# Optimization experiments

Hardware: AMD Instinct MI355X
Metric: run time of the kernel (lower is better)

Reference implementation:

```python
import jax, jax.numpy as jnp
import numpy as np
import math

B, S, T, F_IN, D = 4, 4096, 4096, 127, 64

def setup_inputs() -> dict:
    key = jax.random.key(0)
    k1, k2, k3, k4 = jax.random.split(key, 4)
    return {
        "x1": jax.random.normal(k1, (B, S, F_IN), dtype=jnp.float32),
        "x2": jax.random.normal(k2, (B, T, F_IN), dtype=jnp.float32),
        "W": jax.random.normal(k3, (D, F_IN), dtype=jnp.float32) * (1.0 / math.sqrt(F_IN)),
        "b": jax.random.normal(k4, (D,), dtype=jnp.float32) * 0.01,
    }

def reference(x1, x2, W, b):
    # shared linear projection: torch Linear -> x @ W.T + b
    q = jnp.einsum('bsf,df->bsd', x1, W) + b   # [B,S,D]
    k = jnp.einsum('btf,df->btd', x2, W) + b   # [B,T,D]
    scores = jnp.einsum('bsd,btd->bst', q, k)  # [B,S,T]
    # faithful to source: v4 = v3.div(1/sqrt(D)) == v3 * sqrt(D)
    scores = scores * jnp.sqrt(jnp.float32(D))
    p = jax.nn.softmax(scores, axis=-1)        # [B,S,T]
    # dropout p=0.01 treated as eval-mode identity (deterministic reference)
    out = jnp.einsum('bst,btf->bsf', p, x2)    # [B,S,F_IN]
    return out
```

## Files before the change

### kernel.cpp

```cpp
#include <hip/hip_runtime.h>
#include <hip/hip_bf16.h>


typedef __bf16 bf16x8 __attribute__((ext_vector_type(8)));
typedef float f32x16 __attribute__((ext_vector_type(16)));

#define S_DIM 4096
#define F_DIM 127
#define QSCALE 11.5415603271f
#define THR 11.0f

static __device__ __forceinline__ unsigned short f2bf(float f) {
  unsigned u = __float_as_uint(f);
  unsigned r = u + 0x7FFFu + ((u >> 16) & 1u);
  return (unsigned short)(r >> 16);
}
static __device__ __forceinline__ float bf2f(unsigned short h) {
  return __uint_as_float(((unsigned)h) << 16);
}
static __device__ __forceinline__ unsigned cvt_pk_bf16(float lo, float hi) {
  unsigned r;
  asm("v_cvt_pk_bf16_f32 %0, %1, %2" : "=v"(r) : "v"(lo), "v"(hi));
  return r;
}
static __device__ __forceinline__ float exp2_fast(float x) {
  float r;
  asm("v_exp_f32 %0, %1" : "=v"(r) : "v"(x));
  return r;
}
static __device__ __forceinline__ bf16x8 mk_bf16x8(unsigned w0, unsigned w1,
                                                   unsigned w2, unsigned w3) {
  unsigned t[4] = {w0, w1, w2, w3};
  bf16x8 r;
  __builtin_memcpy(&r, t, 16);
  return r;
}
static __device__ __forceinline__ bf16x8 u4_bf16x8(uint4 v) {
  bf16x8 r;
  __builtin_memcpy(&r, &v, 16);
  return r;
}

__global__ __launch_bounds__(256) void proj_kernel(
    const float* __restrict__ x1, const float* __restrict__ x2,
    const float* __restrict__ W, const float* __restrict__ bias,
    float* __restrict__ Qf, uint4* __restrict__ khf, uint4* __restrict__ klf) {
  __shared__ unsigned kstage[4][32 * 66];
  const int tid = threadIdx.x;
  const int wave = tid >> 6;
  const int lane = tid & 63;
  const int arow = lane & 31;
  const int half = lane >> 5;
  const int bi = blockIdx.x;
  const bool isK = bi >= 128;
  const float* x = isK ? x2 : x1;
  const int grow0 = (bi & 127) * 128 + wave * 32;
  const float* xrow = x + (long)(grow0 + arow) * F_DIM;

  bf16x8 xh[8], xl[8];
#pragma unroll
  for (int kk = 0; kk < 8; ++kk) {
    unsigned short hs[8], ls[8];
#pragma unroll
    for (int j = 0; j < 8; ++j) {
      const int f = kk * 16 + half * 8 + j;
      const float v = (f < F_DIM) ? xrow[f] : 0.f;
      const unsigned short h = f2bf(v);
      hs[j] = h;
      ls[j] = f2bf(v - bf2f(h));
    }
    __builtin_memcpy(&xh[kk], hs, 16);
    __builtin_memcpy(&xl[kk], ls, 16);
  }

  f32x16 acc0, acc1;
#pragma unroll
  for (int r = 0; r < 16; ++r) {
    acc0[r] = 0.f;
    acc1[r] = 0.f;
  }

  const float* wr0 = W + (long)arow * F_DIM;
  const float* wr1 = W + (long)(32 + arow) * F_DIM;
#pragma unroll
  for (int kk = 0; kk < 8; ++kk) {
    unsigned short h0[8], l0[8], h1[8], l1[8];
#pragma unroll
    for (int j = 0; j < 8; ++j) {
      const int f = kk * 16 + half * 8 + j;
      const float v0 = (f < F_DIM) ? wr0[f] : 0.f;
      const float v1 = (f < F_DIM) ? wr1[f] : 0.f;
      const unsigned short a = f2bf(v0);
      h0[j] = a;
      l0[j] = f2bf(v0 - bf2f(a));
      const unsigned short c = f2bf(v1);
      h1[j] = c;
      l1[j] = f2bf(v1 - bf2f(c));
    }
    bf16x8 wh0, wl0, wh1, wl1;
    __builtin_memcpy(&wh0, h0, 16);
    __builtin_memcpy(&wl0, l0, 16);
    __builtin_memcpy(&wh1, h1, 16);
    __builtin_memcpy(&wl1, l1, 16);
    acc0 = __builtin_amdgcn_mfma_f32_32x32x16_bf16(xh[kk], wh0, acc0, 0, 0, 0);
    acc0 = __builtin_amdgcn_mfma_f32_32x32x16_bf16(xh[kk], wl0, acc0, 0, 0, 0);
    acc0 = __builtin_amdgcn_mfma_f32_32x32x16_bf16(xl[kk], wh0, acc0, 0, 0, 0);
    acc1 = __builtin_amdgcn_mfma_f32_32x32x16_bf16(xh[kk], wh1, acc1, 0, 0, 0);
    acc1 = __builtin_amdgcn_mfma_f32_32x32x16_bf16(xh[kk], wl1, acc1, 0, 0, 0);
    acc1 = __builtin_amdgcn_mfma_f32_32x32x16_bf16(xl[kk], wh1, acc1, 0, 0, 0);
  }

  unsigned* kst = kstage[wave];
#pragma unroll
  for (int dt = 0; dt < 2; ++dt) {
    const f32x16 acc = dt ? acc1 : acc0;
    const int d = dt * 32 + arow;
    const float bd = bias[d];
#pragma unroll
    for (int r = 0; r < 16; ++r) {
      const int row = (r & 3) + 8 * (r >> 2) + 4 * half;
      const float val = acc[r] + bd;
      if (!isK) {
        Qf[(long)(grow0 + row) * 64 + d] = val * QSCALE;
      } else {
        const unsigned short h = f2bf(val);
        const unsigned short lo = f2bf(val - bf2f(h));
        kst[row * 66 + d] = (unsigned)h | ((unsigned)lo << 16);
      }
    }
  }

  if (isK) {
    const int b = grow0 >> 12;
    const int tile = (grow0 & (S_DIM - 1)) >> 5;
    uint4* ko = khf + ((long)(b * 128 + tile) * 4) * 64 + lane;
    uint4* lo_ = klf + ((long)(b * 128 + tile) * 4) * 64 + lane;
#pragma unroll
    for (int kk = 0; kk < 4; ++kk) {
      const int d0 = kk * 16 + half * 8;
      unsigned w[8];
#pragma unroll
      for (int j = 0; j < 8; ++j) w[j] = kst[arow * 66 + d0 + j];
      unsigned hw[4], lw[4];
#pragma unroll
      for (int g = 0; g < 4; ++g) {
        hw[g] = (w[2 * g] & 0xffffu) | (w[2 * g + 1] << 16);
        lw[g] = (w[2 * g] >> 16) | (w[2 * g + 1] & 0xffff0000u);
      }
      ko[kk * 64] = make_uint4(hw[0], hw[1], hw[2], hw[3]);
      lo_[kk * 64] = make_uint4(lw[0], lw[1], lw[2], lw[3]);
    }
  }
}

__global__ __launch_bounds__(256) void x2repack_kernel(
    const float* __restrict__ x2, uint4* __restrict__ x2tf) {
  const int tid = threadIdx.x;
  const int bi = blockIdx.x;
  const int b = bi >> 8;
  const int tt = bi & 255;
  const int fb = tid >> 6;
  const int l = tid & 63;
  const int t0 = tt * 16 + ((l >> 5) << 3);
  const int f = fb * 32 + (l & 31);
  const float* src = x2 + ((long)b * S_DIM + t0) * F_DIM + f;
  unsigned short e[8];
#pragma unroll
  for (int j = 0; j < 8; ++j)
    e[j] = (f < F_DIM) ? f2bf(src[(long)j * F_DIM]) : (unsigned short)0;
  unsigned w0 = (unsigned)e[0] | ((unsigned)e[1] << 16);
  unsigned w1 = (unsigned)e[2] | ((unsigned)e[3] << 16);
  unsigned w2 = (unsigned)e[4] | ((unsigned)e[5] << 16);
  unsigned w3 = (unsigned)e[6] | ((unsigned)e[7] << 16);
  x2tf[((long)(b * 256 + tt) * 4 + fb) * 64 + l] = make_uint4(w0, w1, w2, w3);
}

__global__ __launch_bounds__(256, 2) void attn_kernel(
    const float* __restrict__ Qf, const uint4* __restrict__ khf,
    const uint4* __restrict__ klf, const uint4* __restrict__ x2tf,
    float* __restrict__ out) {
  const int tid = threadIdx.x;
  const int lane = tid & 63;
  const int wave = tid >> 6;
  const int col = lane & 31;
  const int half = lane >> 5;
  const int bi = blockIdx.x;
  const int b = bi >> 7;
  const int q0 = (bi & 127) << 5;

  bf16x8 qh[4], ql[4];
  {
    const float* qrow = Qf + ((long)(b * S_DIM + q0 + col)) * 64;
#pragma unroll
    for (int kk = 0; kk < 4; ++kk) {
      const int d0 = kk * 16 + half * 8;
      unsigned short hs[8], ls[8];
#pragma unroll
      for (int j = 0; j < 8; ++j) {
        const float qv = qrow[d0 + j];
        const unsigned short h = f2bf(qv);
        hs[j] = h;
        ls[j] = f2bf(qv - bf2f(h));
      }
      __builtin_memcpy(&qh[kk], hs, 16);
      __builtin_memcpy(&ql[kk], ls, 16);
    }
  }

  const uint4* khfp = khf + (long)b * 128 * 4 * 64;
  const uint4* klfp = klf + (long)b * 128 * 4 * 64;
  const uint4* xfp = x2tf + (long)b * 256 * 4 * 64;

  f32x16 a0, a1, a2, a3;
#pragma unroll
  for (int r = 0; r < 16; ++r) {
    a0[r] = 0.f; a1[r] = 0.f; a2[r] = 0.f; a3[r] = 0.f;
  }
  float m = -INFINITY;
  float lsum = 0.f;

  uint4 KC[8], KN[8];
#pragma unroll
  for (int kk = 0; kk < 4; ++kk) {
    KC[kk] = khfp[(wave * 4 + kk) * 64 + lane];
    KC[4 + kk] = klfp[(wave * 4 + kk) * 64 + lane];
  }

#pragma unroll 2
  for (int it = 0; it < 32; ++it) {
    const int tile = (it << 2) + wave;
    uint4 xv[8];
#pragma unroll
    for (int kf = 0; kf < 2; ++kf)
#pragma unroll
      for (int fb = 0; fb < 4; ++fb)
        xv[kf * 4 + fb] = xfp[((tile * 2 + kf) * 4 + fb) * 64 + lane];
    int tn = tile + 4;
    if (tn > 127) tn = 127;
#pragma unroll
    for (int kk = 0; kk < 4; ++kk) {
      KN[kk] = khfp[(tn * 4 + kk) * 64 + lane];
      KN[4 + kk] = klfp[(tn * 4 + kk) * 64 + lane];
    }
    f32x16 st;
#pragma unroll
    for (int r = 0; r < 16; ++r) st[r] = 0.f;
#pragma unroll
    for (int kk = 0; kk < 4; ++kk) {
      const bf16x8 kv = u4_bf16x8(KC[kk]);
      const bf16x8 lv = u4_bf16x8(KC[4 + kk]);
      st = __builtin_amdgcn_mfma_f32_32x32x16_bf16(kv, qh[kk], st, 0, 0, 0);
      st = __builtin_amdgcn_mfma_f32_32x32x16_bf16(kv, ql[kk], st, 0, 0, 0);
      st = __builtin_amdgcn_mfma_f32_32x32x16_bf16(lv, qh[kk], st, 0, 0, 0);
    }
    float pmax = st[0];
#pragma unroll
    for (int r = 1; r < 16; ++r) pmax = fmaxf(pmax, st[r]);
    pmax = fmaxf(pmax, __shfl_xor(pmax, 32));
    if (__any(pmax > m + THR)) {
      const float mnew = fmaxf(m, pmax);
      const float sc = exp2_fast(m - mnew);
      lsum *= sc;
#pragma unroll
      for (int r = 0; r < 16; ++r) {
        a0[r] *= sc; a1[r] *= sc; a2[r] *= sc; a3[r] *= sc;
      }
      m = mnew;
    }
    float ts = 0.f;
    unsigned pg[4][2];
#pragma unroll
    for (int g = 0; g < 4; ++g) {
      const float p0 = exp2_fast(st[4 * g + 0] - m);
      const float p1 = exp2_fast(st[4 * g + 1] - m);
      const float p2 = exp2_fast(st[4 * g + 2] - m);
      const float p3 = exp2_fast(st[4 * g + 3] - m);
      ts += (p0 + p1) + (p2 + p3);
      pg[g][0] = cvt_pk_bf16(p0, p1);
      pg[g][1] = cvt_pk_bf16(p2, p3);
    }
    lsum += ts;
#pragma unroll
    for (int kk = 0; kk < 2; ++kk) {
      unsigned x0 = pg[2 * kk][0], y0 = pg[2 * kk + 1][0];
      unsigned x1 = pg[2 * kk][1], y1 = pg[2 * kk + 1][1];
      asm("v_permlane32_swap_b32 %0, %1" : "+v"(x0), "+v"(y0));
      asm("v_permlane32_swap_b32 %0, %1" : "+v"(x1), "+v"(y1));
      const bf16x8 pf = mk_bf16x8(x0, x1, y0, y1);
      a0 = __builtin_amdgcn_mfma_f32_32x32x16_bf16(u4_bf16x8(xv[kk * 4 + 0]),
                                                   pf, a0, 0, 0, 0);
      a1 = __builtin_amdgcn_mfma_f32_32x32x16_bf16(u4_bf16x8(xv[kk * 4 + 1]),
                                                   pf, a1, 0, 0, 0);
      a2 = __builtin_amdgcn_mfma_f32_32x32x16_bf16(u4_bf16x8(xv[kk * 4 + 2]),
                                                   pf, a2, 0, 0, 0);
      a3 = __builtin_amdgcn_mfma_f32_32x32x16_bf16(u4_bf16x8(xv[kk * 4 + 3]),
                                                   pf, a3, 0, 0, 0);
    }
#pragma unroll
    for (int i = 0; i < 8; ++i) KC[i] = KN[i];
  }
  lsum += __shfl_xor(lsum, 32);

  __shared__ float mbuf[4][32];
  __shared__ float lbuf[4][32];
  __shared__ float accbuf[128 * 33];
  if (lane < 32) {
    mbuf[wave][col] = m;
    lbuf[wave][col] = lsum;
  }
  __syncthreads();
  const float mstar = fmaxf(fmaxf(mbuf[0][col], mbuf[1][col]),
                            fmaxf(mbuf[2][col], mbuf[3][col]));
  const float wsc = exp2_fast(m - mstar);
  for (int w = 0; w < 4; ++w) {
    if (wave == w) {
#pragma unroll
      for (int fb = 0; fb < 4; ++fb) {
        const f32x16 av = (fb == 0) ? a0 : (fb == 1) ? a1 : (fb == 2) ? a2 : a3;
#pragma unroll
        for (int r = 0; r < 16; ++r) {
          const int f = fb * 32 + (r & 3) + 8 * (r >> 2) + 4 * half;
          const float v = av[r] * wsc;
          if (w == 0) accbuf[f * 33 + col] = v;
          else accbuf[f * 33 + col] += v;
        }
      }
    }
    __syncthreads();
  }
  const int q = tid >> 3;
  const int fg = tid & 7;
  const float ms2 = fmaxf(fmaxf(mbuf[0][q], mbuf[1][q]),
                          fmaxf(mbuf[2][q], mbuf[3][q]));
  float lst = 0.f;
#pragma unroll
  for (int w = 0; w < 4; ++w) lst += lbuf[w][q] * exp2_fast(mbuf[w][q] - ms2);
  const float inv = 1.0f / lst;
  float* ob = out + ((long)(b * S_DIM + q0 + q)) * F_DIM;
#pragma unroll
  for (int j = 0; j < 16; ++j) {
    const int f = fg * 16 + j;
    if (f < F_DIM) ob[f] = accbuf[f * 33 + q] * inv;
  }
}

extern "C" void kernel_launch(void* const* d_in, const int* in_sizes, int n_in,
                              void* d_out, int out_size, void* d_ws,
                              size_t ws_size, hipStream_t stream) {
  const float* x1 = (const float*)d_in[0];
  const float* x2 = (const float*)d_in[1];
  const float* W = (const float*)d_in[2];
  const float* bias = (const float*)d_in[3];
  float* out = (float*)d_out;

  char* ws = (char*)d_ws;
  float* Qf = (float*)ws;
  uint4* khf = (uint4*)(ws + (4l << 20));
  uint4* klf = (uint4*)(ws + (6l << 20));
  uint4* x2tf = (uint4*)(ws + (8l << 20));

  hipLaunchKernelGGL(proj_kernel, dim3(256), dim3(256), 0, stream, x1, x2, W,
                     bias, Qf, khf, klf);
  hipLaunchKernelGGL(x2repack_kernel, dim3(1024), dim3(256), 0, stream, x2,
                     x2tf);
  hipLaunchKernelGGL(attn_kernel, dim3(512), dim3(256), 0, stream, Qf, khf,
                     klf, x2tf, out);
}
```

Before: 76.45 us.

## Prepack W and Q fragments, fold softmax sum into padding column, widen attention blocks

A new kernel pre-splits W into hi/lo bf16 MFMA fragments, stored in the output buffer as scratch, so the projection no longer converts W per block. Q is now written as pre-packed hi/lo bf16 fragments, which removes the per-block split in the attention kernel. The row-sum of probabilities is dropped from the loop: the padded 128th feature column of x2 is set to 1.0, so the PV MFMA computes the denominator for free. The attention kernel uses 512-thread blocks covering 64 queries with an XCD-aware block remap and register double-buffering of K. Together these cut VALU work and conversions, at the cost of a larger reduction LDS footprint and an extra launch.

```diff
diff --git a/kernel.cpp b/kernel.cpp
--- a/kernel.cpp
+++ b/kernel.cpp
@@ -10,14 +10,6 @@
 #define QSCALE 11.5415603271f
 #define THR 11.0f
 
-static __device__ __forceinline__ unsigned short f2bf(float f) {
-  unsigned u = __float_as_uint(f);
-  unsigned r = u + 0x7FFFu + ((u >> 16) & 1u);
-  return (unsigned short)(r >> 16);
-}
-static __device__ __forceinline__ float bf2f(unsigned short h) {
-  return __uint_as_float(((unsigned)h) << 16);
-}
 static __device__ __forceinline__ unsigned cvt_pk_bf16(float lo, float hi) {
   unsigned r;
   asm("v_cvt_pk_bf16_f32 %0, %1, %2" : "=v"(r) : "v"(lo), "v"(hi));
@@ -41,10 +33,36 @@
   return r;
 }
 
+__global__ __launch_bounds__(256) void wfrag_kernel(const float* __restrict__ W,
+                                                    uint4* __restrict__ wf) {
+  const int gid = blockIdx.x * 256 + threadIdx.x;
+  const int dt = gid >> 9;
+  const int kk = (gid >> 6) & 7;
+  const int lane = gid & 63;
+  const int d = dt * 32 + (lane & 31);
+  const int f0b = kk * 16 + (lane >> 5) * 8;
+  const float* wr = W + (long)d * F_DIM;
+  unsigned hw[4], lw[4];
+#pragma unroll
+  for (int g = 0; g < 4; ++g) {
+    const int f0 = f0b + 2 * g;
+    const float v0 = (f0 < F_DIM) ? wr[f0] : 0.f;
+    const float v1 = (f0 + 1 < F_DIM) ? wr[f0 + 1] : 0.f;
+    const unsigned h = cvt_pk_bf16(v0, v1);
+    const float l0 = v0 - __uint_as_float(h << 16);
+    const float l1 = v1 - __uint_as_float(h & 0xffff0000u);
+    hw[g] = h;
+    lw[g] = cvt_pk_bf16(l0, l1);
+  }
+  wf[((dt * 8 + kk) * 64 + lane) * 2 + 0] = make_uint4(hw[0], hw[1], hw[2], hw[3]);
+  wf[((dt * 8 + kk) * 64 + lane) * 2 + 1] = make_uint4(lw[0], lw[1], lw[2], lw[3]);
+}
+
 __global__ __launch_bounds__(256) void proj_kernel(
     const float* __restrict__ x1, const float* __restrict__ x2,
-    const float* __restrict__ W, const float* __restrict__ bias,
-    float* __restrict__ Qf, uint4* __restrict__ khf, uint4* __restrict__ klf) {
+    const uint4* __restrict__ wf, const float* __restrict__ bias,
+    uint4* __restrict__ qhf, uint4* __restrict__ qlf,
+    uint4* __restrict__ khf, uint4* __restrict__ klf) {
   __shared__ unsigned kstage[4][32 * 66];
   const int tid = threadIdx.x;
   const int wave = tid >> 6;
@@ -60,17 +78,20 @@
   bf16x8 xh[8], xl[8];
 #pragma unroll
   for (int kk = 0; kk < 8; ++kk) {
-    unsigned short hs[8], ls[8];
-#pragma unroll
-    for (int j = 0; j < 8; ++j) {
-      const int f = kk * 16 + half * 8 + j;
-      const float v = (f < F_DIM) ? xrow[f] : 0.f;
-      const unsigned short h = f2bf(v);
-      hs[j] = h;
-      ls[j] = f2bf(v - bf2f(h));
-    }
-    __builtin_memcpy(&xh[kk], hs, 16);
-    __builtin_memcpy(&xl[kk], ls, 16);
+    unsigned hw[4], lw[4];
+#pragma unroll
+    for (int g = 0; g < 4; ++g) {
+      const int f0 = kk * 16 + half * 8 + 2 * g;
+      const float v0 = (f0 < F_DIM) ? xrow[f0] : 0.f;
+      const float v1 = (f0 + 1 < F_DIM) ? xrow[f0 + 1] : 0.f;
+      const unsigned h = cvt_pk_bf16(v0, v1);
+      const float l0 = v0 - __uint_as_float(h << 16);
+      const float l1 = v1 - __uint_as_float(h & 0xffff0000u);
+      hw[g] = h;
+      lw[g] = cvt_pk_bf16(l0, l1);
+    }
+    xh[kk] = mk_bf16x8(hw[0], hw[1], hw[2], hw[3]);
+    xl[kk] = mk_bf16x8(lw[0], lw[1], lw[2], lw[3]);
   }
 
   f32x16 acc0, acc1;
@@ -79,29 +100,12 @@
     acc0[r] = 0.f;
     acc1[r] = 0.f;
   }
-
-  const float* wr0 = W + (long)arow * F_DIM;
-  const float* wr1 = W + (long)(32 + arow) * F_DIM;
 #pragma unroll
   for (int kk = 0; kk < 8; ++kk) {
-    unsigned short h0[8], l0[8], h1[8], l1[8];
-#pragma unroll
-    for (int j = 0; j < 8; ++j) {
-      const int f = kk * 16 + half * 8 + j;
-      const float v0 = (f < F_DIM) ? wr0[f] : 0.f;
-      const float v1 = (f < F_DIM) ? wr1[f] : 0.f;
-      const unsigned short a = f2bf(v0);
-      h0[j] = a;
-      l0[j] = f2bf(v0 - bf2f(a));
-      const unsigned short c = f2bf(v1);
-      h1[j] = c;
-      l1[j] = f2bf(v1 - bf2f(c));
-    }
-    bf16x8 wh0, wl0, wh1, wl1;
-    __builtin_memcpy(&wh0, h0, 16);
-    __builtin_memcpy(&wl0, l0, 16);
-    __builtin_memcpy(&wh1, h1, 16);
-    __builtin_memcpy(&wl1, l1, 16);
+    const bf16x8 wh0 = u4_bf16x8(wf[((0 * 8 + kk) * 64 + lane) * 2 + 0]);
+    const bf16x8 wl0 = u4_bf16x8(wf[((0 * 8 + kk) * 64 + lane) * 2 + 1]);
+    const bf16x8 wh1 = u4_bf16x8(wf[((1 * 8 + kk) * 64 + lane) * 2 + 0]);
+    const bf16x8 wl1 = u4_bf16x8(wf[((1 * 8 + kk) * 64 + lane) * 2 + 1]);
     acc0 = __builtin_amdgcn_mfma_f32_32x32x16_bf16(xh[kk], wh0, acc0, 0, 0, 0);
     acc0 = __builtin_amdgcn_mfma_f32_32x32x16_bf16(xh[kk], wl0, acc0, 0, 0, 0);
     acc0 = __builtin_amdgcn_mfma_f32_32x32x16_bf16(xl[kk], wh0, acc0, 0, 0, 0);
@@ -117,39 +121,41 @@
     const int d = dt * 32 + arow;
     const float bd = bias[d];
 #pragma unroll
-    for (int r = 0; r < 16; ++r) {
-      const int row = (r & 3) + 8 * (r >> 2) + 4 * half;
-      const float val = acc[r] + bd;
+    for (int r = 0; r < 16; r += 2) {
+      const int row0 = (r & 3) + 8 * (r >> 2) + 4 * half;
+      float v0 = acc[r] + bd;
+      float v1 = acc[r + 1] + bd;
       if (!isK) {
-        Qf[(long)(grow0 + row) * 64 + d] = val * QSCALE;
-      } else {
-        const unsigned short h = f2bf(val);
-        const unsigned short lo = f2bf(val - bf2f(h));
-        kst[row * 66 + d] = (unsigned)h | ((unsigned)lo << 16);
+        v0 *= QSCALE;
+        v1 *= QSCALE;
       }
-    }
-  }
-
-  if (isK) {
-    const int b = grow0 >> 12;
-    const int tile = (grow0 & (S_DIM - 1)) >> 5;
-    uint4* ko = khf + ((long)(b * 128 + tile) * 4) * 64 + lane;
-    uint4* lo_ = klf + ((long)(b * 128 + tile) * 4) * 64 + lane;
-#pragma unroll
-    for (int kk = 0; kk < 4; ++kk) {
-      const int d0 = kk * 16 + half * 8;
-      unsigned w[8];
-#pragma unroll
-      for (int j = 0; j < 8; ++j) w[j] = kst[arow * 66 + d0 + j];
-      unsigned hw[4], lw[4];
-#pragma unroll
-      for (int g = 0; g < 4; ++g) {
-        hw[g] = (w[2 * g] & 0xffffu) | (w[2 * g + 1] << 16);
-        lw[g] = (w[2 * g] >> 16) | (w[2 * g + 1] & 0xffff0000u);
-      }
-      ko[kk * 64] = make_uint4(hw[0], hw[1], hw[2], hw[3]);
-      lo_[kk * 64] = make_uint4(lw[0], lw[1], lw[2], lw[3]);
-    }
+      const unsigned h = cvt_pk_bf16(v0, v1);
+      const float l0 = v0 - __uint_as_float(h << 16);
+      const float l1 = v1 - __uint_as_float(h & 0xffff0000u);
+      const unsigned l = cvt_pk_bf16(l0, l1);
+      kst[row0 * 66 + d] = (h & 0xffffu) | (l << 16);
+      kst[(row0 + 1) * 66 + d] = (h >> 16) | (l & 0xffff0000u);
+    }
+  }
+
+  const int b = grow0 >> 12;
+  const int tile = (grow0 & (S_DIM - 1)) >> 5;
+  uint4* dh = (isK ? khf : qhf) + ((long)(b * 128 + tile) * 4) * 64 + lane;
+  uint4* dl = (isK ? klf : qlf) + ((long)(b * 128 + tile) * 4) * 64 + lane;
+#pragma unroll
+  for (int kk = 0; kk < 4; ++kk) {
+    const int d0 = kk * 16 + half * 8;
+    unsigned w[8];
+#pragma unroll
+    for (int j = 0; j < 8; ++j) w[j] = kst[arow * 66 + d0 + j];
+    unsigned hw[4], lw[4];
+#pragma unroll
+    for (int g = 0; g < 4; ++g) {
+      hw[g] = (w[2 * g] & 0xffffu) | (w[2 * g + 1] << 16);
+      lw[g] = (w[2 * g] >> 16) | (w[2 * g + 1] & 0xffff0000u);
+    }
+    dh[kk * 64] = make_uint4(hw[0], hw[1], hw[2], hw[3]);
+    dl[kk * 64] = make_uint4(lw[0], lw[1], lw[2], lw[3]);
   }
 }
 
@@ -164,47 +170,40 @@
   const int t0 = tt * 16 + ((l >> 5) << 3);
   const int f = fb * 32 + (l & 31);
   const float* src = x2 + ((long)b * S_DIM + t0) * F_DIM + f;
-  unsigned short e[8];
-#pragma unroll
-  for (int j = 0; j < 8; ++j)
-    e[j] = (f < F_DIM) ? f2bf(src[(long)j * F_DIM]) : (unsigned short)0;
-  unsigned w0 = (unsigned)e[0] | ((unsigned)e[1] << 16);
-  unsigned w1 = (unsigned)e[2] | ((unsigned)e[3] << 16);
-  unsigned w2 = (unsigned)e[4] | ((unsigned)e[5] << 16);
-  unsigned w3 = (unsigned)e[6] | ((unsigned)e[7] << 16);
-  x2tf[((long)(b * 256 + tt) * 4 + fb) * 64 + l] = make_uint4(w0, w1, w2, w3);
-}
-
-__global__ __launch_bounds__(256, 2) void attn_kernel(
-    const float* __restrict__ Qf, const uint4* __restrict__ khf,
-    const uint4* __restrict__ klf, const uint4* __restrict__ x2tf,
-    float* __restrict__ out) {
+  unsigned w[4];
+#pragma unroll
+  for (int g = 0; g < 4; ++g) {
+    const float v0 = (f < F_DIM) ? src[(long)(2 * g) * F_DIM] : 1.0f;
+    const float v1 = (f < F_DIM) ? src[(long)(2 * g + 1) * F_DIM] : 1.0f;
+    w[g] = cvt_pk_bf16(v0, v1);
+  }
+  x2tf[((long)(b * 256 + tt) * 4 + fb) * 64 + l] = make_uint4(w[0], w[1], w[2], w[3]);
+}
+
+__global__ __launch_bounds__(512, 2) void attn_kernel(
+    const uint4* __restrict__ qhf, const uint4* __restrict__ qlf,
+    const uint4* __restrict__ khf, const uint4* __restrict__ klf,
+    const uint4* __restrict__ x2tf, float* __restrict__ out) {
   const int tid = threadIdx.x;
   const int lane = tid & 63;
   const int wave = tid >> 6;
   const int col = lane & 31;
   const int half = lane >> 5;
+  const int sub = wave & 1;
+  const int qtr = wave >> 1;
   const int bi = blockIdx.x;
-  const int b = bi >> 7;
-  const int q0 = (bi & 127) << 5;
-
+  const int xcd = bi & 7;
+  const int slot = bi >> 3;
+  const int L = (xcd >> 1) * 64 + slot * 2 + (xcd & 1);
+  const int b = L >> 6;
+  const int q0 = (L & 63) << 6;
+
+  const int qtile = ((q0 + sub * 32) & (S_DIM - 1)) >> 5;
   bf16x8 qh[4], ql[4];
-  {
-    const float* qrow = Qf + ((long)(b * S_DIM + q0 + col)) * 64;
-#pragma unroll
-    for (int kk = 0; kk < 4; ++kk) {
-      const int d0 = kk * 16 + half * 8;
-      unsigned short hs[8], ls[8];
-#pragma unroll
-      for (int j = 0; j < 8; ++j) {
-        const float qv = qrow[d0 + j];
-        const unsigned short h = f2bf(qv);
-        hs[j] = h;
-        ls[j] = f2bf(qv - bf2f(h));
-      }
-      __builtin_memcpy(&qh[kk], hs, 16);
-      __builtin_memcpy(&ql[kk], ls, 16);
-    }
+#pragma unroll
+  for (int kk = 0; kk < 4; ++kk) {
+    qh[kk] = u4_bf16x8(qhf[((long)(b * 128 + qtile) * 4 + kk) * 64 + lane]);
+    ql[kk] = u4_bf16x8(qlf[((long)(b * 128 + qtile) * 4 + kk) * 64 + lane]);
   }
 
   const uint4* khfp = khf + (long)b * 128 * 4 * 64;
@@ -217,38 +216,40 @@
     a0[r] = 0.f; a1[r] = 0.f; a2[r] = 0.f; a3[r] = 0.f;
   }
   float m = -INFINITY;
-  float lsum = 0.f;
-
-  uint4 KC[8], KN[8];
-#pragma unroll
-  for (int kk = 0; kk < 4; ++kk) {
-    KC[kk] = khfp[(wave * 4 + kk) * 64 + lane];
-    KC[4 + kk] = klfp[(wave * 4 + kk) * 64 + lane];
-  }
-
-#pragma unroll 2
-  for (int it = 0; it < 32; ++it) {
-    const int tile = (it << 2) + wave;
+
+  uint4 KA[8], KB[8];
+  {
+    const int t0_ = qtr;
+#pragma unroll
+    for (int kk = 0; kk < 4; ++kk) {
+      KA[kk] = khfp[(t0_ * 4 + kk) * 64 + lane];
+      KA[4 + kk] = klfp[(t0_ * 4 + kk) * 64 + lane];
+    }
+  }
+
+  auto body = [&](const uint4 (&C)[8], uint4 (&N)[8], int i) {
+    const int tile = (i << 2) + qtr;
     uint4 xv[8];
 #pragma unroll
     for (int kf = 0; kf < 2; ++kf)
 #pragma unroll
       for (int fb = 0; fb < 4; ++fb)
         xv[kf * 4 + fb] = xfp[((tile * 2 + kf) * 4 + fb) * 64 + lane];
-    int tn = tile + 4;
-    if (tn > 127) tn = 127;
+    if (i < 31) {
+      const int tn = ((i + 1) << 2) + qtr;
+#pragma unroll
+      for (int kk = 0; kk < 4; ++kk) {
+        N[kk] = khfp[(tn * 4 + kk) * 64 + lane];
+        N[4 + kk] = klfp[(tn * 4 + kk) * 64 + lane];
+      }
+    }
+    f32x16 st;
+#pragma unroll
+    for (int r = 0; r < 16; ++r) st[r] = 0.f;
 #pragma unroll
     for (int kk = 0; kk < 4; ++kk) {
-      KN[kk] = khfp[(tn * 4 + kk) * 64 + lane];
-      KN[4 + kk] = klfp[(tn * 4 + kk) * 64 + lane];
-    }
-    f32x16 st;
-#pragma unroll
-    for (int r = 0; r < 16; ++r) st[r] = 0.f;
-#pragma unroll
-    for (int kk = 0; kk < 4; ++kk) {
-      const bf16x8 kv = u4_bf16x8(KC[kk]);
-      const bf16x8 lv = u4_bf16x8(KC[4 + kk]);
+      const bf16x8 kv = u4_bf16x8(C[kk]);
+      const bf16x8 lv = u4_bf16x8(C[4 + kk]);
       st = __builtin_amdgcn_mfma_f32_32x32x16_bf16(kv, qh[kk], st, 0, 0, 0);
       st = __builtin_amdgcn_mfma_f32_32x32x16_bf16(kv, ql[kk], st, 0, 0, 0);
       st = __builtin_amdgcn_mfma_f32_32x32x16_bf16(lv, qh[kk], st, 0, 0, 0);
@@ -260,26 +261,20 @@
     if (__any(pmax > m + THR)) {
       const float mnew = fmaxf(m, pmax);
       const float sc = exp2_fast(m - mnew);
-      lsum *= sc;
 #pragma unroll
       for (int r = 0; r < 16; ++r) {
         a0[r] *= sc; a1[r] *= sc; a2[r] *= sc; a3[r] *= sc;
       }
       m = mnew;
     }
-    float ts = 0.f;
     unsigned pg[4][2];
 #pragma unroll
     for (int g = 0; g < 4; ++g) {
-      const float p0 = exp2_fast(st[4 * g + 0] - m);
-      const float p1 = exp2_fast(st[4 * g + 1] - m);
-      const float p2 = exp2_fast(st[4 * g + 2] - m);
-      const float p3 = exp2_fast(st[4 * g + 3] - m);
-      ts += (p0 + p1) + (p2 + p3);
-      pg[g][0] = cvt_pk_bf16(p0, p1);
-      pg[g][1] = cvt_pk_bf16(p2, p3);
-    }
-    lsum += ts;
+      pg[g][0] = cvt_pk_bf16(exp2_fast(st[4 * g + 0] - m),
+                             exp2_fast(st[4 * g + 1] - m));
+      pg[g][1] = cvt_pk_bf16(exp2_fast(st[4 * g + 2] - m),
+                             exp2_fast(st[4 * g + 3] - m));
+    }
 #pragma unroll
     for (int kk = 0; kk < 2; ++kk) {
       unsigned x0 = pg[2 * kk][0], y0 = pg[2 * kk + 1][0];
@@ -296,51 +291,52 @@
       a3 = __builtin_amdgcn_mfma_f32_32x32x16_bf16(u4_bf16x8(xv[kk * 4 + 3]),
                                                    pf, a3, 0, 0, 0);
     }
-#pragma unroll
-    for (int i = 0; i < 8; ++i) KC[i] = KN[i];
-  }
-  lsum += __shfl_xor(lsum, 32);
-
-  __shared__ float mbuf[4][32];
-  __shared__ float lbuf[4][32];
-  __shared__ float accbuf[128 * 33];
-  if (lane < 32) {
-    mbuf[wave][col] = m;
-    lbuf[wave][col] = lsum;
-  }
+  };
+
+  for (int i = 0; i < 32; i += 2) {
+    body(KA, KB, i);
+    body(KB, KA, i + 1);
+  }
+
+  __shared__ float mbuf[8][32];
+  __shared__ float accb[2][128 * 33];
+  if (lane < 32) mbuf[wave][col] = m;
   __syncthreads();
-  const float mstar = fmaxf(fmaxf(mbuf[0][col], mbuf[1][col]),
-                            fmaxf(mbuf[2][col], mbuf[3][col]));
+  float mstar = mbuf[sub][col];
+#pragma unroll
+  for (int w = 1; w < 4; ++w) mstar = fmaxf(mstar, mbuf[sub + 2 * w][col]);
   const float wsc = exp2_fast(m - mstar);
-  for (int w = 0; w < 4; ++w) {
-    if (wave == w) {
-#pragma unroll
-      for (int fb = 0; fb < 4; ++fb) {
-        const f32x16 av = (fb == 0) ? a0 : (fb == 1) ? a1 : (fb == 2) ? a2 : a3;
-#pragma unroll
-        for (int r = 0; r < 16; ++r) {
-          const int f = fb * 32 + (r & 3) + 8 * (r >> 2) + 4 * half;
-          const float v = av[r] * wsc;
-          if (w == 0) accbuf[f * 33 + col] = v;
-          else accbuf[f * 33 + col] += v;
-        }
-      }
+  float* buf = accb[sub];
+  auto emit = [&](const f32x16& av, int fb, bool first) {
+#pragma unroll
+    for (int r = 0; r < 16; ++r) {
+      const int f = fb * 32 + (r & 3) + 8 * (r >> 2) + 4 * half;
+      const float v = av[r] * wsc;
+      if (first) buf[f * 33 + col] = v;
+      else buf[f * 33 + col] += v;
+    }
+  };
+  for (int p = 0; p < 4; ++p) {
+    if (qtr == p) {
+      const bool first = (p == 0);
+      emit(a0, 0, first);
+      emit(a1, 1, first);
+      emit(a2, 2, first);
+      emit(a3, 3, first);
     }
     __syncthreads();
   }
-  const int q = tid >> 3;
+
+  const int q64 = tid >> 3;
   const int fg = tid & 7;
-  const float ms2 = fmaxf(fmaxf(mbuf[0][q], mbuf[1][q]),
-                          fmaxf(mbuf[2][q], mbuf[3][q]));
-  float lst = 0.f;
-#pragma unroll
-  for (int w = 0; w < 4; ++w) lst += lbuf[w][q] * exp2_fast(mbuf[w][q] - ms2);
-  const float inv = 1.0f / lst;
-  float* ob = out + ((long)(b * S_DIM + q0 + q)) * F_DIM;
+  const int s2 = q64 >> 5;
+  const int qq = q64 & 31;
+  const float inv = 1.0f / accb[s2][127 * 33 + qq];
+  float* ob = out + ((long)(b * S_DIM + q0 + q64)) * F_DIM;
 #pragma unroll
   for (int j = 0; j < 16; ++j) {
     const int f = fg * 16 + j;
-    if (f < F_DIM) ob[f] = accbuf[f * 33 + q] * inv;
+    if (f < F_DIM) ob[f] = accb[s2][f * 33 + qq] * inv;
   }
 }
 
@@ -354,15 +350,18 @@
   float* out = (float*)d_out;
 
   char* ws = (char*)d_ws;
-  float* Qf = (float*)ws;
+  uint4* qhf = (uint4*)ws;
+  uint4* qlf = (uint4*)(ws + (2l << 20));
   uint4* khf = (uint4*)(ws + (4l << 20));
   uint4* klf = (uint4*)(ws + (6l << 20));
   uint4* x2tf = (uint4*)(ws + (8l << 20));
-
-  hipLaunchKernelGGL(proj_kernel, dim3(256), dim3(256), 0, stream, x1, x2, W,
-                     bias, Qf, khf, klf);
+  uint4* wf = (uint4*)d_out;
+
+  hipLaunchKernelGGL(wfrag_kernel, dim3(4), dim3(256), 0, stream, W, wf);
+  hipLaunchKernelGGL(proj_kernel, dim3(256), dim3(256), 0, stream, x1, x2, wf,
+                     bias, qhf, qlf, khf, klf);
   hipLaunchKernelGGL(x2repack_kernel, dim3(1024), dim3(256), 0, stream, x2,
                      x2tf);
-  hipLaunchKernelGGL(attn_kernel, dim3(512), dim3(256), 0, stream, Qf, khf,
-                     klf, x2tf, out);
-}
+  hipLaunchKernelGGL(attn_kernel, dim3(256), dim3(512), 0, stream, qhf, qlf,
+                     khf, klf, x2tf, out);
+}
```

Measured after the change: 77.79 us. About the same (+1.8%).
